# Kernel optimization log

Measured on AMD Instinct MI355X. Metric: run time of the kernel, lower is better.

## Reference

```python
import jax, jax.numpy as jnp
import numpy as np

EPS = 1e-5

def _conv(x, w, pad):
    # NCHW conv, stride 1, no bias
    return jax.lax.conv_general_dilated(x, w, (1, 1), [(pad, pad), (pad, pad)],
                                        dimension_numbers=('NCHW', 'OIHW', 'NCHW'))

def _bn(x, g, b, m, v):
    # inference-mode BatchNorm2d folded to scale/shift
    s = g * jax.lax.rsqrt(v + EPS)
    return x * s[None, :, None, None] + (b - m * s)[None, :, None, None]

def _cbr(x, w, g, b, m, v):
    # convolution helper module: 3x3 conv (pad 1, no bias) + BN + ReLU
    return jax.nn.relu(_bn(_conv(x, w, 1), g, b, m, v))


def setup_inputs() -> dict:
    key = jax.random.key(0)
    ks = iter(jax.random.split(key, 40))
    dim, mid, B, H, W = 256, 128, 4, 128, 128
    def conv_w(shape):
        fan = shape[1] * shape[2] * shape[3]
        return jax.random.normal(next(ks), shape, jnp.float32) / np.float32(np.sqrt(fan))
    def bn_p(c):
        return (jax.random.normal(next(ks), (c,), jnp.float32) * 0.1 + 1.0,
                jax.random.normal(next(ks), (c,), jnp.float32) * 0.1,
                jax.random.normal(next(ks), (c,), jnp.float32) * 0.1,
                jax.random.uniform(next(ks), (c,), jnp.float32, 0.5, 1.5))
    x = jax.random.normal(next(ks), (B, dim, H, W), jnp.float32)
    w_p1 = conv_w((mid, dim, 3, 3)); g_p1, b_p1, m_p1, v_p1 = bn_p(mid)
    w_p2 = conv_w((mid, dim, 3, 3)); g_p2, b_p2, m_p2, v_p2 = bn_p(mid)
    w_pc = conv_w((dim, mid, 3, 3)); g_pb, b_pb, m_pb, v_pb = bn_p(dim)
    w_c1 = conv_w((dim, dim, 1, 1)); g_b1, b_b1, m_b1, v_b1 = bn_p(dim)
    w_c2 = conv_w((dim, dim, 3, 3)); g_c2, b_c2, m_c2, v_c2 = bn_p(dim)
    return dict(x=x,
                w_p1=w_p1, g_p1=g_p1, b_p1=b_p1, m_p1=m_p1, v_p1=v_p1,
                w_p2=w_p2, g_p2=g_p2, b_p2=b_p2, m_p2=m_p2, v_p2=v_p2,
                w_pc=w_pc, g_pb=g_pb, b_pb=b_pb, m_pb=m_pb, v_pb=v_pb,
                w_c1=w_c1, g_b1=g_b1, b_b1=b_b1, m_b1=m_b1, v_b1=v_b1,
                w_c2=w_c2, g_c2=g_c2, b_c2=b_c2, m_c2=m_c2, v_c2=v_c2)


def reference(x, w_p1, g_p1, b_p1, m_p1, v_p1,
              w_p2, g_p2, b_p2, m_p2, v_p2,
              w_pc, g_pb, b_pb, m_pb, v_pb,
              w_c1, g_b1, b_b1, m_b1, v_b1,
              w_c2, g_c2, b_c2, m_c2, v_c2):
    p1 = _cbr(x, w_p1, g_p1, b_p1, m_p1, v_p1)          # [B,128,H,W]
    top = jax.lax.cummax(p1, axis=2, reverse=True)       # TopPool: max over rows below
    p2 = _cbr(x, w_p2, g_p2, b_p2, m_p2, v_p2)          # [B,128,H,W]
    left = jax.lax.cummax(p2, axis=3, reverse=True)      # LeftPool: max over cols to the right
    p_bn1 = _bn(_conv(top + left, w_pc, 1), g_pb, b_pb, m_pb, v_pb)  # [B,dim,H,W]
    bn1 = _bn(_conv(x, w_c1, 0), g_b1, b_b1, m_b1, v_b1)             # 1x1 skip branch
    relu1 = jax.nn.relu(p_bn1 + bn1)
    return _cbr(relu1, w_c2, g_c2, b_c2, m_c2, v_c2)
```

## Files before the change

kernel.cpp:

```cpp
#include <hip/hip_runtime.h>
#include <hip/hip_bf16.h>

#define HH 128
#define WW 128
#define BB 4
#define NPIX 16384
#define EPSV 1e-5f

using bfrag = __attribute__((ext_vector_type(8))) short;
using f32x4 = __attribute__((ext_vector_type(4))) float;
using us8   = __attribute__((ext_vector_type(8))) unsigned short;

__device__ __forceinline__ float bf2f(ushort u) {
  union { unsigned int i; float f; } x; x.i = ((unsigned int)u) << 16; return x.f;
}
__device__ __forceinline__ ushort f2bf(float f) {
  union { float f; unsigned int i; } x; x.f = f;
  unsigned int r = x.i + 0x7fffu + ((x.i >> 16) & 1u);
  return (ushort)(r >> 16);
}

#define GLOAD16(gsrc, ldst) \
  __builtin_amdgcn_global_load_lds( \
      (const __attribute__((address_space(1))) unsigned int*)(gsrc), \
      (__attribute__((address_space(3))) unsigned int*)(ldst), 16, 0, 0)

template<int CIN1, int TAPS1, int CIN2, int TAPS2, int EPI>
__global__ __launch_bounds__(256, 2)
void convgemm(const ushort* __restrict__ B1,
              const ushort* __restrict__ B2,
              const ushort* __restrict__ wR,
              const float*  __restrict__ tb,
              const float*  __restrict__ tb2,
              void*          __restrict__ outp,
              const ushort* __restrict__ zerop)
{
  __shared__ ushort lds[2][16384];
  constexpr int nch1 = CIN1 / 64;
  constexpr int nch2 = (CIN2 > 0) ? CIN2 / 64 : 0;
  constexpr int NCH  = TAPS1 * nch1 + TAPS2 * nch2;

  const int g  = blockIdx.x & 7;
  const int r  = blockIdx.x >> 3;
  const int bo = r >> 4;
  const int h  = g * 16 + (r & 15);
  const int o_base = (bo & 1) * 128;
  const int b  = bo >> 1;

  const int tid  = threadIdx.x;
  const int lane = tid & 63;
  const int wid  = tid >> 6;
  const int m0 = (wid >> 1) * 64;
  const int n0 = (wid & 1) * 64;

  f32x4 acc[4][4];
  #pragma unroll
  for (int i = 0; i < 4; ++i)
    #pragma unroll
    for (int j = 0; j < 4; ++j) acc[i][j] = (f32x4){0.f, 0.f, 0.f, 0.f};

  int rowB[4], ro1[4], ro2[4];
  #pragma unroll
  for (int s = 0; s < 4; ++s) {
    const int boff = (wid * 4 + s) * 1024 + lane * 16;
    rowB[s] = boff >> 7;
    const int sl8 = ((((boff >> 4) & 7) ^ (rowB[s] & 7)) << 3);
    ro1[s] = rowB[s] * CIN1 + sl8;
    ro2[s] = (CIN2 > 0) ? rowB[s] * CIN2 + sl8 : 0;
  }
  const size_t B1base = (size_t)b * NPIX * CIN1;
  const size_t B2base = (CIN2 > 0) ? (size_t)b * NPIX * CIN2 : 0;

  auto stage = [&](int t, int buf) {
    char* base = (char*)&lds[buf][0];
    const ushort* wsrc = wR + ((size_t)t * 256 + o_base) * 64;
    const ushort* bch;
    int zr; bool oob, ph2;
    if (CIN2 == 0 || t < TAPS1 * nch1) {
      const int tap = t / nch1, ch = t - tap * nch1;
      const int dy = (TAPS1 == 9) ? tap / 3 - 1 : 0;
      const int dx = (TAPS1 == 9) ? tap - (tap / 3) * 3 - 1 : 0;
      const int hy = h + dy;
      oob = (hy < 0) | (hy >= HH);
      zr  = (dx < 0) ? 0 : ((dx > 0) ? 127 : -1);
      bch = B1 + B1base + (size_t)(hy * WW + dx) * CIN1 + ch * 64;
      ph2 = false;
    } else {
      const int ch = t - TAPS1 * nch1;
      oob = false; zr = -1;
      bch = B2 + B2base + (size_t)(h * WW) * CIN2 + ch * 64;
      ph2 = true;
    }
    #pragma unroll
    for (int s = 0; s < 4; ++s) {
      const int off = (wid * 4 + s) * 1024;
      GLOAD16((const char*)wsrc + off + lane * 16, base + off);
      const int roff = ph2 ? ro2[s] : ro1[s];
      const ushort* bs = (oob || rowB[s] == zr) ? zerop : (bch + roff);
      GLOAD16(bs, base + 16384 + off);
    }
  };

  auto compute = [&](int buf) {
    const char* base = (const char*)&lds[buf][0];
    bfrag af[2][4], bfv[2][4];
    #pragma unroll
    for (int kc = 0; kc < 2; ++kc) {
      const int sw = ((((kc << 2) | (lane >> 4)) ^ (lane & 7)) << 4);
      #pragma unroll
      for (int mf = 0; mf < 4; ++mf)
        af[kc][mf] = *(const bfrag*)(base + (m0 + mf * 16 + (lane & 15)) * 128 + sw);
      #pragma unroll
      for (int nf = 0; nf < 4; ++nf)
        bfv[kc][nf] = *(const bfrag*)(base + 16384 + (n0 + nf * 16 + (lane & 15)) * 128 + sw);
    }
    __builtin_amdgcn_s_setprio(1);
    #pragma unroll
    for (int kc = 0; kc < 2; ++kc)
      #pragma unroll
      for (int mf = 0; mf < 4; ++mf)
        #pragma unroll
        for (int nf = 0; nf < 4; ++nf)
          acc[mf][nf] = __builtin_amdgcn_mfma_f32_16x16x32_bf16(
              af[kc][mf], bfv[kc][nf], acc[mf][nf], 0, 0, 0);
    __builtin_amdgcn_s_setprio(0);
  };

  stage(0, 0);
  int cur = 0;
  for (int t = 0; t < NCH; ++t) {
    asm volatile("s_waitcnt vmcnt(0)" ::: "memory");
    __builtin_amdgcn_s_barrier();
    __builtin_amdgcn_sched_barrier(0);
    if (t + 1 < NCH) stage(t + 1, cur ^ 1);
    compute(cur);
    cur ^= 1;
  }

  if (EPI == 4) {
    __syncthreads();
    ushort* ct = (ushort*)&lds[0][0];
    const int pl0 = n0 + (lane & 15);
    #pragma unroll
    for (int mf = 0; mf < 4; ++mf) {
      #pragma unroll
      for (int r2 = 0; r2 < 4; ++r2) {
        const int ol = m0 + mf * 16 + (lane >> 4) * 4 + r2;
        const int o  = o_base + ol;
        const float bias = tb[o] + tb2[o];
        #pragma unroll
        for (int nf = 0; nf < 4; ++nf)
          ct[(pl0 + nf * 16) * 136 + ol] =
              f2bf(fmaxf(acc[mf][nf][r2] + bias, 0.f));
      }
    }
    __syncthreads();
    const int p  = tid >> 1;
    const int hf = tid & 1;
    ushort* dst = (ushort*)outp +
                  ((size_t)b * NPIX + h * WW + p) * 256 + o_base + hf * 64;
    const ushort* src = ct + p * 136 + hf * 64;
    #pragma unroll
    for (int j = 0; j < 8; ++j)
      *(us8*)(dst + j * 8) = *(const us8*)(src + j * 8);
    return;
  }

  const int pc0 = h * WW + n0 + (lane & 15);
  #pragma unroll
  for (int mf = 0; mf < 4; ++mf) {
    #pragma unroll
    for (int r2 = 0; r2 < 4; ++r2) {
      const int o = o_base + m0 + mf * 16 + (lane >> 4) * 4 + r2;
      const float bias = tb[o];
      #pragma unroll
      for (int nf = 0; nf < 4; ++nf) {
        const int p = pc0 + nf * 16;
        float v = fmaxf(acc[mf][nf][r2] + bias, 0.f);
        const size_t oi = ((size_t)(b * 256 + o)) * NPIX + p;
        if (EPI == 0) ((ushort*)outp)[oi] = f2bf(v);
        else          ((float*)outp)[oi] = v;
      }
    }
  }
}

struct WSeg {
  const float *W, *g, *bb, *mm, *vv;
  ushort* dst; float* tb;
  int CIN, COUT, TAPS, o_off, cb, start, end;
};

__device__ __forceinline__ void wrepack_one(const WSeg& s, int e) {
  const int tap = e % s.TAPS;
  const int ci  = (e / s.TAPS) % s.CIN;
  const int o   = e / (s.TAPS * s.CIN);
  const int oi  = o + s.o_off;
  const float sc = s.g[o] * rsqrtf(s.vv[o] + EPSV);
  const int nch = s.CIN / 64;
  const int ch = ci >> 6, kl = ci & 63;
  const int slot = (kl >> 3) ^ (oi & 7);
  s.dst[(((size_t)((s.cb + tap * nch + ch) * s.COUT) + oi) << 6) +
        (slot << 3) + (kl & 7)] = f2bf(s.W[e] * sc);
  if (ci == 0 && tap == 0) s.tb[oi] = s.bb[o] - s.mm[o] * sc;
}

__global__ __launch_bounds__(256)
void wrepack_all(WSeg s0, WSeg s1, WSeg s2, WSeg s3, WSeg s4) {
  const int id = blockIdx.x * 256 + threadIdx.x;
  if (id < s0.end)      wrepack_one(s0, id - s0.start);
  else if (id < s1.end) wrepack_one(s1, id - s1.start);
  else if (id < s2.end) wrepack_one(s2, id - s2.start);
  else if (id < s3.end) wrepack_one(s3, id - s3.start);
  else if (id < s4.end) wrepack_one(s4, id - s4.start);
}

__global__ __launch_bounds__(256)
void repack_x(const float* __restrict__ x, ushort* __restrict__ xT)
{
  const int b  = blockIdx.z;
  const int cq = threadIdx.x >> 6;
  const int pg = threadIdx.x & 63;
  const int p0 = blockIdx.x * 256 + pg * 4;
  const size_t xb = (size_t)b * 256 * NPIX;
  ushort* ob = xT + ((size_t)b * NPIX + p0) * 256 + cq * 64;
  for (int cc = 0; cc < 64; cc += 8) {
    us8 v[4];
    #pragma unroll
    for (int j = 0; j < 8; ++j) {
      const float4 q = *(const float4*)&x[xb + (size_t)(cq * 64 + cc + j) * NPIX + p0];
      v[0][j] = f2bf(q.x); v[1][j] = f2bf(q.y);
      v[2][j] = f2bf(q.z); v[3][j] = f2bf(q.w);
    }
    #pragma unroll
    for (int k = 0; k < 4; ++k)
      *(us8*)(ob + (size_t)k * 256 + cc) = v[k];
  }
}

__global__ __launch_bounds__(256)
void sum_repack(const ushort* __restrict__ p12, ushort* __restrict__ sT)
{
  const int b  = blockIdx.z;
  const int cq = threadIdx.x >> 6;
  const int pg = threadIdx.x & 63;
  const int p0 = blockIdx.x * 256 + pg * 4;
  const size_t base = (size_t)b * 256 * NPIX;
  const ushort* P1 = p12 + base;
  const ushort* P2 = p12 + base + (size_t)128 * NPIX;
  ushort* ob = sT + ((size_t)b * NPIX + p0) * 128 + cq * 32;
  for (int cc = 0; cc < 32; cc += 8) {
    us8 v[4];
    #pragma unroll
    for (int j = 0; j < 8; ++j) {
      const size_t ci = (size_t)(cq * 32 + cc + j) * NPIX + p0;
      const ushort4 a = *(const ushort4*)&P1[ci];
      const ushort4 d = *(const ushort4*)&P2[ci];
      v[0][j] = f2bf(bf2f(a.x) + bf2f(d.x));
      v[1][j] = f2bf(bf2f(a.y) + bf2f(d.y));
      v[2][j] = f2bf(bf2f(a.z) + bf2f(d.z));
      v[3][j] = f2bf(bf2f(a.w) + bf2f(d.w));
    }
    #pragma unroll
    for (int k = 0; k < 4; ++k)
      *(us8*)(ob + (size_t)k * 128 + cc) = v[k];
  }
}

__global__ __launch_bounds__(256)
void scans(ushort* __restrict__ p)
{
  const int bid = blockIdx.x;
  if (bid < 256) {
    const int b = bid >> 6;
    const int c = (bid & 63) * 2 + (threadIdx.x >> 7);
    const int w = threadIdx.x & 127;
    ushort* base = p + ((size_t)(b * 256 + c)) * NPIX + w;
    float cur = bf2f(base[(HH - 1) * WW]);
    for (int hr = HH - 2; hr >= 0; --hr) {
      cur = fmaxf(cur, bf2f(base[hr * WW]));
      base[hr * WW] = f2bf(cur);
    }
  } else {
    const int lane = threadIdx.x & 63;
    const int rid  = (bid - 256) * 4 + (threadIdx.x >> 6);
    const int b = rid >> 14;
    const int rem = rid & 16383;
    const int c = rem >> 7, h = rem & 127;
    ushort* r = p + ((size_t)(b * 256 + 128 + c)) * NPIX + h * WW;
    const ushort2 u = ((const ushort2*)r)[lane];
    const float e0 = bf2f(u.x), e1 = bf2f(u.y);
    float m = fmaxf(e0, e1);
    #pragma unroll
    for (int off = 1; off < 64; off <<= 1) {
      const float o = __shfl_down(m, off, 64);
      if (lane + off < 64) m = fmaxf(m, o);
    }
    float s = __shfl_down(m, 1, 64);
    if (lane == 63) s = -3.4e38f;
    const float o1 = fmaxf(e1, s);
    const float o0 = fmaxf(e0, o1);
    ushort2 w2; w2.x = f2bf(o0); w2.y = f2bf(o1);
    ((ushort2*)r)[lane] = w2;
  }
}

extern "C" void kernel_launch(void* const* d_in, const int* in_sizes, int n_in,
                              void* d_out, int out_size, void* d_ws, size_t ws_size,
                              hipStream_t stream) {
  const float* x    = (const float*)d_in[0];
  const float* w_p1 = (const float*)d_in[1];
  const float* g_p1 = (const float*)d_in[2];
  const float* b_p1 = (const float*)d_in[3];
  const float* m_p1 = (const float*)d_in[4];
  const float* v_p1 = (const float*)d_in[5];
  const float* w_p2 = (const float*)d_in[6];
  const float* g_p2 = (const float*)d_in[7];
  const float* b_p2 = (const float*)d_in[8];
  const float* m_p2 = (const float*)d_in[9];
  const float* v_p2 = (const float*)d_in[10];
  const float* w_pc = (const float*)d_in[11];
  const float* g_pb = (const float*)d_in[12];
  const float* b_pb = (const float*)d_in[13];
  const float* m_pb = (const float*)d_in[14];
  const float* v_pb = (const float*)d_in[15];
  const float* w_c1 = (const float*)d_in[16];
  const float* g_b1 = (const float*)d_in[17];
  const float* b_b1 = (const float*)d_in[18];
  const float* m_b1 = (const float*)d_in[19];
  const float* v_b1 = (const float*)d_in[20];
  const float* w_c2 = (const float*)d_in[21];
  const float* g_c2 = (const float*)d_in[22];
  const float* b_c2 = (const float*)d_in[23];
  const float* m_c2 = (const float*)d_in[24];
  const float* v_c2 = (const float*)d_in[25];

  char* ws = (char*)d_ws;
  ushort* xT      = (ushort*)(ws + 0);
  ushort* p12     = (ushort*)(ws + 33554432);
  ushort* relu1T  = (ushort*)(ws + 33554432);
  ushort* sumT    = (ushort*)(ws + 67108864);
  ushort* wR_p12  = (ushort*)(ws + 100663296);
  ushort* wR_pcc1 = (ushort*)(ws + 101842944);
  ushort* wR_c2   = (ushort*)(ws + 102563840);
  float*  tb_p12  = (float*)(ws + 103743488);
  float*  tb_pc   = (float*)(ws + 103744512);
  float*  tb_c1   = (float*)(ws + 103745536);
  float*  tb_c2   = (float*)(ws + 103746560);
  ushort* zerop   = (ushort*)(ws + 103747584);

  hipMemsetAsync(zerop, 0, 256, stream);

  const int n_p  = 128 * 256 * 9;
  const int n_pc = 256 * 128 * 9;
  const int n_c1 = 256 * 256 * 1;
  const int n_c2 = 256 * 256 * 9;
  WSeg s0 = {w_p1, g_p1, b_p1, m_p1, v_p1, wR_p12, tb_p12, 256, 256, 9, 0, 0,
             0, n_p};
  WSeg s1 = {w_p2, g_p2, b_p2, m_p2, v_p2, wR_p12, tb_p12, 256, 256, 9, 128, 0,
             n_p, 2 * n_p};
  WSeg s2 = {w_pc, g_pb, b_pb, m_pb, v_pb, wR_pcc1, tb_pc, 128, 256, 9, 0, 0,
             2 * n_p, 2 * n_p + n_pc};
  WSeg s3 = {w_c1, g_b1, b_b1, m_b1, v_b1, wR_pcc1, tb_c1, 256, 256, 1, 0, 18,
             2 * n_p + n_pc, 2 * n_p + n_pc + n_c1};
  WSeg s4 = {w_c2, g_c2, b_c2, m_c2, v_c2, wR_c2, tb_c2, 256, 256, 9, 0, 0,
             2 * n_p + n_pc + n_c1, 2 * n_p + n_pc + n_c1 + n_c2};
  const int n_all = 2 * n_p + n_pc + n_c1 + n_c2;
  wrepack_all<<<dim3((n_all + 255) / 256), 256, 0, stream>>>(s0, s1, s2, s3, s4);

  repack_x<<<dim3(NPIX / 256, 1, BB), 256, 0, stream>>>(x, xT);

  convgemm<256, 9, 0, 0, 0><<<dim3(1024), 256, 0, stream>>>(
      xT, nullptr, wR_p12, tb_p12, nullptr, p12, zerop);

  scans<<<dim3(256 + 16384), 256, 0, stream>>>(p12);

  sum_repack<<<dim3(NPIX / 256, 1, BB), 256, 0, stream>>>(p12, sumT);

  convgemm<128, 9, 256, 1, 4><<<dim3(1024), 256, 0, stream>>>(
      sumT, xT, wR_pcc1, tb_pc, tb_c1, relu1T, zerop);

  convgemm<256, 9, 0, 0, 3><<<dim3(1024), 256, 0, stream>>>(
      relu1T, nullptr, wR_c2, tb_c2, nullptr, (void*)d_out, zerop);
}
```

Before: 300.2 us.

## Enlarge conv GEMM tile to 256 outputs x 2 rows with 512-thread blocks

Each convgemm block now computes all 256 output channels for two image rows (256 pixels) with 8 waves, and each wave holds a 128x64 accumulator tile. This halves redundant loads: weights are staged once per block instead of per half, and activations are reused across all output channels. Weight and activation staging is split into two phases, interleaved with the two MFMA halves and partial vmcnt waits, to overlap loads with compute. The larger LDS footprint (128KB) and doubled accumulators raise register and LDS pressure and cut the grid to 256 blocks, which lowers occupancy.

```diff
diff --git a/kernel.cpp b/kernel.cpp
--- a/kernel.cpp
+++ b/kernel.cpp
@@ -26,7 +26,7 @@
       (__attribute__((address_space(3))) unsigned int*)(ldst), 16, 0, 0)
 
 template<int CIN1, int TAPS1, int CIN2, int TAPS2, int EPI>
-__global__ __launch_bounds__(256, 2)
+__global__ __launch_bounds__(512, 2)
 void convgemm(const ushort* __restrict__ B1,
               const ushort* __restrict__ B2,
               const ushort* __restrict__ wR,
@@ -35,85 +35,98 @@
               void*          __restrict__ outp,
               const ushort* __restrict__ zerop)
 {
-  __shared__ ushort lds[2][16384];
+  __shared__ char ldsb[131072];
   constexpr int nch1 = CIN1 / 64;
   constexpr int nch2 = (CIN2 > 0) ? CIN2 / 64 : 0;
   constexpr int NCH  = TAPS1 * nch1 + TAPS2 * nch2;
 
-  const int g  = blockIdx.x & 7;
-  const int r  = blockIdx.x >> 3;
-  const int bo = r >> 4;
-  const int h  = g * 16 + (r & 15);
-  const int o_base = (bo & 1) * 128;
-  const int b  = bo >> 1;
+  const int nid = (blockIdx.x & 7) * 32 + (blockIdx.x >> 3);
+  const int b   = nid >> 6;
+  const int h2  = (nid & 63) * 2;
 
   const int tid  = threadIdx.x;
   const int lane = tid & 63;
   const int wid  = tid >> 6;
-  const int m0 = (wid >> 1) * 64;
-  const int n0 = (wid & 1) * 64;
-
-  f32x4 acc[4][4];
+  const int wc   = wid & 3;
+  const int m0   = (wid >> 2) * 128;
+  const int n0   = wc * 64;
+
+  f32x4 acc[8][4];
   #pragma unroll
-  for (int i = 0; i < 4; ++i)
+  for (int i = 0; i < 8; ++i)
     #pragma unroll
     for (int j = 0; j < 4; ++j) acc[i][j] = (f32x4){0.f, 0.f, 0.f, 0.f};
 
-  int rowB[4], ro1[4], ro2[4];
+  const int sl8 = (((tid & 7) ^ ((tid >> 3) & 7)) << 3);
+  int ro1[4], ro2[4], w_[4], prow_[4];
   #pragma unroll
   for (int s = 0; s < 4; ++s) {
-    const int boff = (wid * 4 + s) * 1024 + lane * 16;
-    rowB[s] = boff >> 7;
-    const int sl8 = ((((boff >> 4) & 7) ^ (rowB[s] & 7)) << 3);
-    ro1[s] = rowB[s] * CIN1 + sl8;
-    ro2[s] = (CIN2 > 0) ? rowB[s] * CIN2 + sl8 : 0;
+    const int rowB = s * 64 + (tid >> 3);
+    prow_[s] = rowB >> 7;
+    w_[s]    = rowB & 127;
+    ro1[s]   = (prow_[s] * WW + w_[s]) * CIN1 + sl8;
+    ro2[s]   = (CIN2 > 0) ? rowB * CIN2 + sl8 : 0;
   }
   const size_t B1base = (size_t)b * NPIX * CIN1;
   const size_t B2base = (CIN2 > 0) ? (size_t)b * NPIX * CIN2 : 0;
 
-  auto stage = [&](int t, int buf) {
-    char* base = (char*)&lds[buf][0];
-    const ushort* wsrc = wR + ((size_t)t * 256 + o_base) * 64;
-    const ushort* bch;
-    int zr; bool oob, ph2;
+  auto stageB = [&](int t, int buf) {
+    char* base = ldsb + buf * 65536 + 32768;
     if (CIN2 == 0 || t < TAPS1 * nch1) {
       const int tap = t / nch1, ch = t - tap * nch1;
       const int dy = (TAPS1 == 9) ? tap / 3 - 1 : 0;
       const int dx = (TAPS1 == 9) ? tap - (tap / 3) * 3 - 1 : 0;
-      const int hy = h + dy;
-      oob = (hy < 0) | (hy >= HH);
-      zr  = (dx < 0) ? 0 : ((dx > 0) ? 127 : -1);
-      bch = B1 + B1base + (size_t)(hy * WW + dx) * CIN1 + ch * 64;
-      ph2 = false;
+      const int hy0 = h2 + dy;
+      const bool oob0 = (hy0 < 0) | (hy0 > 127);
+      const bool oob1 = (hy0 + 1 < 0) | (hy0 + 1 > 127);
+      const int zr = (dx < 0) ? 0 : ((dx > 0) ? 127 : -1);
+      const ushort* bch = B1 + B1base + (size_t)(hy0 * WW + dx) * CIN1 + ch * 64;
+      #pragma unroll
+      for (int s = 0; s < 4; ++s) {
+        const bool bad = (prow_[s] ? oob1 : oob0) || (w_[s] == zr);
+        const ushort* src = bad ? zerop : (bch + ro1[s]);
+        GLOAD16(src, base + s * 8192 + tid * 16);
+      }
     } else {
       const int ch = t - TAPS1 * nch1;
-      oob = false; zr = -1;
-      bch = B2 + B2base + (size_t)(h * WW) * CIN2 + ch * 64;
-      ph2 = true;
-    }
-    #pragma unroll
-    for (int s = 0; s < 4; ++s) {
-      const int off = (wid * 4 + s) * 1024;
-      GLOAD16((const char*)wsrc + off + lane * 16, base + off);
-      const int roff = ph2 ? ro2[s] : ro1[s];
-      const ushort* bs = (oob || rowB[s] == zr) ? zerop : (bch + roff);
-      GLOAD16(bs, base + 16384 + off);
+      const ushort* bch = B2 + B2base + (size_t)(h2 * WW) * CIN2 + ch * 64;
+      #pragma unroll
+      for (int s = 0; s < 4; ++s)
+        GLOAD16(bch + ro2[s], base + s * 8192 + tid * 16);
     }
   };
 
-  auto compute = [&](int buf) {
-    const char* base = (const char*)&lds[buf][0];
-    bfrag af[2][4], bfv[2][4];
+  auto stageA = [&](int t, int buf) {
+    char* base = ldsb + buf * 65536;
+    const char* wsrc = (const char*)(wR + (size_t)t * (256 * 64));
+    GLOAD16(wsrc + 0 * 8192 + tid * 16, base + 0 * 8192 + tid * 16);
+    GLOAD16(wsrc + 2 * 8192 + tid * 16, base + 2 * 8192 + tid * 16);
+    GLOAD16(wsrc + 1 * 8192 + tid * 16, base + 1 * 8192 + tid * 16);
+    GLOAD16(wsrc + 3 * 8192 + tid * 16, base + 3 * 8192 + tid * 16);
+  };
+
+  stageB(0, 0);
+  stageA(0, 0);
+  int cur = 0;
+  for (int t = 0; t < NCH; ++t) {
+    const char* cbase = ldsb + cur * 65536;
+    asm volatile("s_waitcnt vmcnt(2)" ::: "memory");
+    __builtin_amdgcn_s_barrier();
+    __builtin_amdgcn_sched_barrier(0);
+    bfrag bf[2][4], af[2][4];
     #pragma unroll
     for (int kc = 0; kc < 2; ++kc) {
       const int sw = ((((kc << 2) | (lane >> 4)) ^ (lane & 7)) << 4);
       #pragma unroll
+      for (int nf = 0; nf < 4; ++nf)
+        bf[kc][nf] = *(const bfrag*)(cbase + 32768 +
+                        (n0 + nf * 16 + (lane & 15)) * 128 + sw);
+      #pragma unroll
       for (int mf = 0; mf < 4; ++mf)
-        af[kc][mf] = *(const bfrag*)(base + (m0 + mf * 16 + (lane & 15)) * 128 + sw);
-      #pragma unroll
-      for (int nf = 0; nf < 4; ++nf)
-        bfv[kc][nf] = *(const bfrag*)(base + 16384 + (n0 + nf * 16 + (lane & 15)) * 128 + sw);
-    }
+        af[kc][mf] = *(const bfrag*)(cbase +
+                        (m0 + mf * 16 + (lane & 15)) * 128 + sw);
+    }
+    if (t + 1 < NCH) stageB(t + 1, cur ^ 1);
     __builtin_amdgcn_s_setprio(1);
     #pragma unroll
     for (int kc = 0; kc < 2; ++kc)
@@ -122,62 +135,84 @@
         #pragma unroll
         for (int nf = 0; nf < 4; ++nf)
           acc[mf][nf] = __builtin_amdgcn_mfma_f32_16x16x32_bf16(
-              af[kc][mf], bfv[kc][nf], acc[mf][nf], 0, 0, 0);
+              af[kc][mf], bf[kc][nf], acc[mf][nf], 0, 0, 0);
     __builtin_amdgcn_s_setprio(0);
-  };
-
-  stage(0, 0);
-  int cur = 0;
-  for (int t = 0; t < NCH; ++t) {
-    asm volatile("s_waitcnt vmcnt(0)" ::: "memory");
+    __builtin_amdgcn_sched_barrier(0);
+    if (t + 1 < NCH) asm volatile("s_waitcnt vmcnt(4)" ::: "memory");
+    else             asm volatile("s_waitcnt vmcnt(0)" ::: "memory");
     __builtin_amdgcn_s_barrier();
     __builtin_amdgcn_sched_barrier(0);
-    if (t + 1 < NCH) stage(t + 1, cur ^ 1);
-    compute(cur);
-    cur ^= 1;
-  }
-
-  if (EPI == 4) {
-    __syncthreads();
-    ushort* ct = (ushort*)&lds[0][0];
-    const int pl0 = n0 + (lane & 15);
-    #pragma unroll
-    for (int mf = 0; mf < 4; ++mf) {
-      #pragma unroll
-      for (int r2 = 0; r2 < 4; ++r2) {
-        const int ol = m0 + mf * 16 + (lane >> 4) * 4 + r2;
-        const int o  = o_base + ol;
-        const float bias = tb[o] + tb2[o];
+    bfrag ag[2][4];
+    #pragma unroll
+    for (int kc = 0; kc < 2; ++kc) {
+      const int sw = ((((kc << 2) | (lane >> 4)) ^ (lane & 7)) << 4);
+      #pragma unroll
+      for (int mf = 0; mf < 4; ++mf)
+        ag[kc][mf] = *(const bfrag*)(cbase +
+                        (m0 + 64 + mf * 16 + (lane & 15)) * 128 + sw);
+    }
+    if (t + 1 < NCH) stageA(t + 1, cur ^ 1);
+    __builtin_amdgcn_s_setprio(1);
+    #pragma unroll
+    for (int kc = 0; kc < 2; ++kc)
+      #pragma unroll
+      for (int mf = 0; mf < 4; ++mf)
         #pragma unroll
         for (int nf = 0; nf < 4; ++nf)
-          ct[(pl0 + nf * 16) * 136 + ol] =
-              f2bf(fmaxf(acc[mf][nf][r2] + bias, 0.f));
+          acc[4 + mf][nf] = __builtin_amdgcn_mfma_f32_16x16x32_bf16(
+              ag[kc][mf], bf[kc][nf], acc[4 + mf][nf], 0, 0, 0);
+    __builtin_amdgcn_s_setprio(0);
+    __builtin_amdgcn_sched_barrier(0);
+    cur ^= 1;
+  }
+
+  if (EPI == 4) {
+    ushort* ct = (ushort*)ldsb;
+    #pragma unroll
+    for (int ph = 0; ph < 2; ++ph) {
+      __syncthreads();
+      if ((wc >> 1) == ph) {
+        const int lp0 = (wc & 1) * 64 + (lane & 15);
+        #pragma unroll
+        for (int mf = 0; mf < 8; ++mf) {
+          #pragma unroll
+          for (int r2 = 0; r2 < 4; ++r2) {
+            const int o = m0 + mf * 16 + (lane >> 4) * 4 + r2;
+            const float bias = tb[o] + tb2[o];
+            #pragma unroll
+            for (int nf = 0; nf < 4; ++nf)
+              ct[(lp0 + nf * 16) * 264 + o] =
+                  f2bf(fmaxf(acc[mf][nf][r2] + bias, 0.f));
+          }
+        }
       }
-    }
-    __syncthreads();
-    const int p  = tid >> 1;
-    const int hf = tid & 1;
-    ushort* dst = (ushort*)outp +
-                  ((size_t)b * NPIX + h * WW + p) * 256 + o_base + hf * 64;
-    const ushort* src = ct + p * 136 + hf * 64;
-    #pragma unroll
-    for (int j = 0; j < 8; ++j)
-      *(us8*)(dst + j * 8) = *(const us8*)(src + j * 8);
+      __syncthreads();
+      const int lp = tid >> 2;
+      const int q  = tid & 3;
+      ushort* dst = (ushort*)outp +
+          ((size_t)b * NPIX + (h2 + ph) * WW + lp) * 256 + q * 64;
+      const ushort* src = ct + lp * 264 + q * 64;
+      #pragma unroll
+      for (int j = 0; j < 8; ++j)
+        *(us8*)(dst + j * 8) = *(const us8*)(src + j * 8);
+    }
     return;
   }
 
-  const int pc0 = h * WW + n0 + (lane & 15);
+  const int prow = wc >> 1;
+  const int hout = h2 + prow;
+  const int wbase = (wc & 1) * 64 + (lane & 15);
   #pragma unroll
-  for (int mf = 0; mf < 4; ++mf) {
+  for (int mf = 0; mf < 8; ++mf) {
     #pragma unroll
     for (int r2 = 0; r2 < 4; ++r2) {
-      const int o = o_base + m0 + mf * 16 + (lane >> 4) * 4 + r2;
+      const int o = m0 + mf * 16 + (lane >> 4) * 4 + r2;
       const float bias = tb[o];
       #pragma unroll
       for (int nf = 0; nf < 4; ++nf) {
-        const int p = pc0 + nf * 16;
+        const int w = wbase + nf * 16;
         float v = fmaxf(acc[mf][nf][r2] + bias, 0.f);
-        const size_t oi = ((size_t)(b * 256 + o)) * NPIX + p;
+        const size_t oi = (((size_t)(b * 256 + o)) << 14) + hout * WW + w;
         if (EPI == 0) ((ushort*)outp)[oi] = f2bf(v);
         else          ((float*)outp)[oi] = v;
       }
@@ -370,16 +405,16 @@
 
   repack_x<<<dim3(NPIX / 256, 1, BB), 256, 0, stream>>>(x, xT);
 
-  convgemm<256, 9, 0, 0, 0><<<dim3(1024), 256, 0, stream>>>(
+  convgemm<256, 9, 0, 0, 0><<<dim3(256), 512, 0, stream>>>(
       xT, nullptr, wR_p12, tb_p12, nullptr, p12, zerop);
 
   scans<<<dim3(256 + 16384), 256, 0, stream>>>(p12);
 
   sum_repack<<<dim3(NPIX / 256, 1, BB), 256, 0, stream>>>(p12, sumT);
 
-  convgemm<128, 9, 256, 1, 4><<<dim3(1024), 256, 0, stream>>>(
+  convgemm<128, 9, 256, 1, 4><<<dim3(256), 512, 0, stream>>>(
       sumT, xT, wR_pcc1, tb_pc, tb_c1, relu1T, zerop);
 
-  convgemm<256, 9, 0, 0, 3><<<dim3(1024), 256, 0, stream>>>(
+  convgemm<256, 9, 0, 0, 3><<<dim3(256), 512, 0, stream>>>(
       relu1T, nullptr, wR_c2, tb_c2, nullptr, (void*)d_out, zerop);
 }
```

Result: faster. 287.1 us (-4.4%).

## Load weight fragments straight to registers and deepen activation LDS pipeline

Applied to the files above, without the earlier changes.

Weight (A) fragments for the next K-chunk are now loaded from global memory directly into registers, double-buffered across two register sets, instead of being staged through LDS. Activation (B) tiles are staged two chunks ahead into a 4-slot LDS ring, with partial vmcnt waits in place of full drains. The goal is to remove LDS traffic and bank pressure for the weights and to hide global latency behind more MFMA work. In exchange it raises register pressure, duplicates weight reads across waves that share m0, and makes the vmcnt counting fragile.

```diff
diff --git a/kernel.cpp b/kernel.cpp
--- a/kernel.cpp
+++ b/kernel.cpp
@@ -35,7 +35,7 @@
               void*          __restrict__ outp,
               const ushort* __restrict__ zerop)
 {
-  __shared__ ushort lds[2][16384];
+  __shared__ ushort lds[4][8192];
   constexpr int nch1 = CIN1 / 64;
   constexpr int nch2 = (CIN2 > 0) ? CIN2 / 64 : 0;
   constexpr int NCH  = TAPS1 * nch1 + TAPS2 * nch2;
@@ -62,7 +62,7 @@
   int rowB[4], ro1[4], ro2[4];
   #pragma unroll
   for (int s = 0; s < 4; ++s) {
-    const int boff = (wid * 4 + s) * 1024 + lane * 16;
+    const int boff = s * 4096 + tid * 16;
     rowB[s] = boff >> 7;
     const int sl8 = ((((boff >> 4) & 7) ^ (rowB[s] & 7)) << 3);
     ro1[s] = rowB[s] * CIN1 + sl8;
@@ -71,11 +71,9 @@
   const size_t B1base = (size_t)b * NPIX * CIN1;
   const size_t B2base = (CIN2 > 0) ? (size_t)b * NPIX * CIN2 : 0;
 
-  auto stage = [&](int t, int buf) {
+  auto stageB = [&](int t, int buf) {
     char* base = (char*)&lds[buf][0];
-    const ushort* wsrc = wR + ((size_t)t * 256 + o_base) * 64;
-    const ushort* bch;
-    int zr; bool oob, ph2;
+    const ushort* bch; int zr; bool oob, ph2;
     if (CIN2 == 0 || t < TAPS1 * nch1) {
       const int tap = t / nch1, ch = t - tap * nch1;
       const int dy = (TAPS1 == 9) ? tap / 3 - 1 : 0;
@@ -93,48 +91,63 @@
     }
     #pragma unroll
     for (int s = 0; s < 4; ++s) {
-      const int off = (wid * 4 + s) * 1024;
-      GLOAD16((const char*)wsrc + off + lane * 16, base + off);
       const int roff = ph2 ? ro2[s] : ro1[s];
       const ushort* bs = (oob || rowB[s] == zr) ? zerop : (bch + roff);
-      GLOAD16(bs, base + 16384 + off);
+      GLOAD16(bs, base + s * 4096 + tid * 16);
     }
   };
 
-  auto compute = [&](int buf) {
-    const char* base = (const char*)&lds[buf][0];
-    bfrag af[2][4], bfv[2][4];
-    #pragma unroll
-    for (int kc = 0; kc < 2; ++kc) {
-      const int sw = ((((kc << 2) | (lane >> 4)) ^ (lane & 7)) << 4);
-      #pragma unroll
-      for (int mf = 0; mf < 4; ++mf)
-        af[kc][mf] = *(const bfrag*)(base + (m0 + mf * 16 + (lane & 15)) * 128 + sw);
-      #pragma unroll
-      for (int nf = 0; nf < 4; ++nf)
-        bfv[kc][nf] = *(const bfrag*)(base + 16384 + (n0 + nf * 16 + (lane & 15)) * 128 + sw);
-    }
-    __builtin_amdgcn_s_setprio(1);
-    #pragma unroll
-    for (int kc = 0; kc < 2; ++kc)
-      #pragma unroll
-      for (int mf = 0; mf < 4; ++mf)
-        #pragma unroll
-        for (int nf = 0; nf < 4; ++nf)
-          acc[mf][nf] = __builtin_amdgcn_mfma_f32_16x16x32_bf16(
-              af[kc][mf], bfv[kc][nf], acc[mf][nf], 0, 0, 0);
-    __builtin_amdgcn_s_setprio(0);
-  };
-
-  stage(0, 0);
-  int cur = 0;
-  for (int t = 0; t < NCH; ++t) {
-    asm volatile("s_waitcnt vmcnt(0)" ::: "memory");
-    __builtin_amdgcn_s_barrier();
-    __builtin_amdgcn_sched_barrier(0);
-    if (t + 1 < NCH) stage(t + 1, cur ^ 1);
-    compute(cur);
-    cur ^= 1;
+#define LOADA(t_, A_) do { \
+    const char* wsrc_ = (const char*)wR + (size_t)(t_) * 32768 + \
+                        (size_t)(o_base + m0 + (lane & 15)) * 128; \
+    _Pragma("unroll") \
+    for (int kc_ = 0; kc_ < 2; ++kc_) { \
+      const int sw_ = ((((kc_ << 2) | (lane >> 4)) ^ (lane & 7)) << 4); \
+      _Pragma("unroll") \
+      for (int mf_ = 0; mf_ < 4; ++mf_) \
+        A_[kc_][mf_] = *(const bfrag*)(wsrc_ + mf_ * 2048 + sw_); \
+    } } while (0)
+
+#define BODY(t_, Acur_, Anext_) do { \
+    if ((t_) + 1 < NCH) { asm volatile("s_waitcnt vmcnt(12)" ::: "memory"); } \
+    else                { asm volatile("s_waitcnt vmcnt(8)"  ::: "memory"); } \
+    __builtin_amdgcn_s_barrier(); \
+    __builtin_amdgcn_sched_barrier(0); \
+    if ((t_) + 1 < NCH) LOADA((t_) + 1, Anext_); \
+    __builtin_amdgcn_sched_barrier(0); \
+    if ((t_) + 2 < NCH) stageB((t_) + 2, ((t_) + 2) & 3); \
+    const char* bbase_ = (const char*)&lds[(t_) & 3][0]; \
+    bfrag bf_[2][4]; \
+    _Pragma("unroll") \
+    for (int kc_ = 0; kc_ < 2; ++kc_) { \
+      const int sw_ = ((((kc_ << 2) | (lane >> 4)) ^ (lane & 7)) << 4); \
+      _Pragma("unroll") \
+      for (int nf_ = 0; nf_ < 4; ++nf_) \
+        bf_[kc_][nf_] = *(const bfrag*)(bbase_ + \
+                          (n0 + nf_ * 16 + (lane & 15)) * 128 + sw_); \
+    } \
+    __builtin_amdgcn_s_setprio(1); \
+    _Pragma("unroll") \
+    for (int kc_ = 0; kc_ < 2; ++kc_) \
+      _Pragma("unroll") \
+      for (int mf_ = 0; mf_ < 4; ++mf_) \
+        _Pragma("unroll") \
+        for (int nf_ = 0; nf_ < 4; ++nf_) \
+          acc[mf_][nf_] = __builtin_amdgcn_mfma_f32_16x16x32_bf16( \
+              Acur_[kc_][mf_], bf_[kc_][nf_], acc[mf_][nf_], 0, 0, 0); \
+    __builtin_amdgcn_s_setprio(0); \
+    __builtin_amdgcn_sched_barrier(0); \
+  } while (0)
+
+  bfrag Aa[2][4], Ab[2][4];
+  stageB(0, 0);
+  __builtin_amdgcn_sched_barrier(0);
+  LOADA(0, Aa);
+  __builtin_amdgcn_sched_barrier(0);
+  stageB(1, 1);
+  for (int t = 0; t < NCH; t += 2) {
+    BODY(t, Aa, Ab);
+    BODY(t + 1, Ab, Aa);
   }
 
   if (EPI == 4) {
@@ -183,6 +196,8 @@
       }
     }
   }
+#undef BODY
+#undef LOADA
 }
 
 struct WSeg {
```

Measured after the change: 342.5 us. 14.1% more time.

## Emit pool convs channel-last and fuse scans with sum into transposed buffers

Applied to the files above, without the earlier changes.

The first pool conv now writes its output in pixel-major (channel-last) layout through the EPI 4 epilogue, using a zero second bias. This replaces the in-place NCHW scans and the separate sum_repack transpose with two scan kernels: one runs the top cummax into a topT buffer, the other runs the left cummax and adds topT directly into sumT. The GEMM loop is also reordered so the LDS fragment reads happen before the next stage's global loads are issued. The new scans use only 512 blocks of 128 threads, each running a serial loop of 128 steps, so parallelism is low, and topT adds an extra buffer round trip.

```diff
diff --git a/kernel.cpp b/kernel.cpp
--- a/kernel.cpp
+++ b/kernel.cpp
@@ -101,8 +101,13 @@
     }
   };
 
-  auto compute = [&](int buf) {
-    const char* base = (const char*)&lds[buf][0];
+  stage(0, 0);
+  int cur = 0;
+  for (int t = 0; t < NCH; ++t) {
+    asm volatile("s_waitcnt vmcnt(0)" ::: "memory");
+    __builtin_amdgcn_s_barrier();
+    __builtin_amdgcn_sched_barrier(0);
+    const char* base = (const char*)&lds[cur][0];
     bfrag af[2][4], bfv[2][4];
     #pragma unroll
     for (int kc = 0; kc < 2; ++kc) {
@@ -114,6 +119,7 @@
       for (int nf = 0; nf < 4; ++nf)
         bfv[kc][nf] = *(const bfrag*)(base + 16384 + (n0 + nf * 16 + (lane & 15)) * 128 + sw);
     }
+    if (t + 1 < NCH) stage(t + 1, cur ^ 1);
     __builtin_amdgcn_s_setprio(1);
     #pragma unroll
     for (int kc = 0; kc < 2; ++kc)
@@ -124,16 +130,6 @@
           acc[mf][nf] = __builtin_amdgcn_mfma_f32_16x16x32_bf16(
               af[kc][mf], bfv[kc][nf], acc[mf][nf], 0, 0, 0);
     __builtin_amdgcn_s_setprio(0);
-  };
-
-  stage(0, 0);
-  int cur = 0;
-  for (int t = 0; t < NCH; ++t) {
-    asm volatile("s_waitcnt vmcnt(0)" ::: "memory");
-    __builtin_amdgcn_s_barrier();
-    __builtin_amdgcn_sched_barrier(0);
-    if (t + 1 < NCH) stage(t + 1, cur ^ 1);
-    compute(cur);
     cur ^= 1;
   }
 
@@ -238,70 +234,35 @@
   }
 }
 
-__global__ __launch_bounds__(256)
-void sum_repack(const ushort* __restrict__ p12, ushort* __restrict__ sT)
+__global__ __launch_bounds__(128)
+void scan_top(const ushort* __restrict__ p12T, ushort* __restrict__ topT)
 {
-  const int b  = blockIdx.z;
-  const int cq = threadIdx.x >> 6;
-  const int pg = threadIdx.x & 63;
-  const int p0 = blockIdx.x * 256 + pg * 4;
-  const size_t base = (size_t)b * 256 * NPIX;
-  const ushort* P1 = p12 + base;
-  const ushort* P2 = p12 + base + (size_t)128 * NPIX;
-  ushort* ob = sT + ((size_t)b * NPIX + p0) * 128 + cq * 32;
-  for (int cc = 0; cc < 32; cc += 8) {
-    us8 v[4];
-    #pragma unroll
-    for (int j = 0; j < 8; ++j) {
-      const size_t ci = (size_t)(cq * 32 + cc + j) * NPIX + p0;
-      const ushort4 a = *(const ushort4*)&P1[ci];
-      const ushort4 d = *(const ushort4*)&P2[ci];
-      v[0][j] = f2bf(bf2f(a.x) + bf2f(d.x));
-      v[1][j] = f2bf(bf2f(a.y) + bf2f(d.y));
-      v[2][j] = f2bf(bf2f(a.z) + bf2f(d.z));
-      v[3][j] = f2bf(bf2f(a.w) + bf2f(d.w));
-    }
-    #pragma unroll
-    for (int k = 0; k < 4; ++k)
-      *(us8*)(ob + (size_t)k * 128 + cc) = v[k];
-  }
-}
-
-__global__ __launch_bounds__(256)
-void scans(ushort* __restrict__ p)
+  const int b = blockIdx.x >> 7;
+  const int w = blockIdx.x & 127;
+  const int c = threadIdx.x;
+  const size_t ib = (size_t)b * NPIX;
+  float cur = -3.4e38f;
+  for (int h = HH - 1; h >= 0; --h) {
+    const size_t p = ib + h * WW + w;
+    cur = fmaxf(cur, bf2f(p12T[p * 256 + c]));
+    topT[p * 128 + c] = f2bf(cur);
+  }
+}
+
+__global__ __launch_bounds__(128)
+void scan_left_sum(const ushort* __restrict__ p12T,
+                   const ushort* __restrict__ topT,
+                   ushort* __restrict__ sumT)
 {
-  const int bid = blockIdx.x;
-  if (bid < 256) {
-    const int b = bid >> 6;
-    const int c = (bid & 63) * 2 + (threadIdx.x >> 7);
-    const int w = threadIdx.x & 127;
-    ushort* base = p + ((size_t)(b * 256 + c)) * NPIX + w;
-    float cur = bf2f(base[(HH - 1) * WW]);
-    for (int hr = HH - 2; hr >= 0; --hr) {
-      cur = fmaxf(cur, bf2f(base[hr * WW]));
-      base[hr * WW] = f2bf(cur);
-    }
-  } else {
-    const int lane = threadIdx.x & 63;
-    const int rid  = (bid - 256) * 4 + (threadIdx.x >> 6);
-    const int b = rid >> 14;
-    const int rem = rid & 16383;
-    const int c = rem >> 7, h = rem & 127;
-    ushort* r = p + ((size_t)(b * 256 + 128 + c)) * NPIX + h * WW;
-    const ushort2 u = ((const ushort2*)r)[lane];
-    const float e0 = bf2f(u.x), e1 = bf2f(u.y);
-    float m = fmaxf(e0, e1);
-    #pragma unroll
-    for (int off = 1; off < 64; off <<= 1) {
-      const float o = __shfl_down(m, off, 64);
-      if (lane + off < 64) m = fmaxf(m, o);
-    }
-    float s = __shfl_down(m, 1, 64);
-    if (lane == 63) s = -3.4e38f;
-    const float o1 = fmaxf(e1, s);
-    const float o0 = fmaxf(e0, o1);
-    ushort2 w2; w2.x = f2bf(o0); w2.y = f2bf(o1);
-    ((ushort2*)r)[lane] = w2;
+  const int b = blockIdx.x >> 7;
+  const int h = blockIdx.x & 127;
+  const int c = threadIdx.x;
+  const size_t ib = (size_t)b * NPIX + h * WW;
+  float cur = -3.4e38f;
+  for (int w = WW - 1; w >= 0; --w) {
+    const size_t p = ib + w;
+    cur = fmaxf(cur, bf2f(p12T[p * 256 + 128 + c]));
+    sumT[p * 128 + c] = f2bf(cur + bf2f(topT[p * 128 + c]));
   }
 }
 
@@ -337,9 +298,10 @@
 
   char* ws = (char*)d_ws;
   ushort* xT      = (ushort*)(ws + 0);
-  ushort* p12     = (ushort*)(ws + 33554432);
+  ushort* p12T    = (ushort*)(ws + 33554432);
   ushort* relu1T  = (ushort*)(ws + 33554432);
   ushort* sumT    = (ushort*)(ws + 67108864);
+  ushort* topT    = (ushort*)(ws + 83886080);
   ushort* wR_p12  = (ushort*)(ws + 100663296);
   ushort* wR_pcc1 = (ushort*)(ws + 101842944);
   ushort* wR_c2   = (ushort*)(ws + 102563840);
@@ -348,8 +310,9 @@
   float*  tb_c1   = (float*)(ws + 103745536);
   float*  tb_c2   = (float*)(ws + 103746560);
   ushort* zerop   = (ushort*)(ws + 103747584);
-
-  hipMemsetAsync(zerop, 0, 256, stream);
+  float*  tb_zero = (float*)(ws + 103747840);
+
+  hipMemsetAsync(zerop, 0, 256 + 1024, stream);
 
   const int n_p  = 128 * 256 * 9;
   const int n_pc = 256 * 128 * 9;
@@ -370,12 +333,11 @@
 
   repack_x<<<dim3(NPIX / 256, 1, BB), 256, 0, stream>>>(x, xT);
 
-  convgemm<256, 9, 0, 0, 0><<<dim3(1024), 256, 0, stream>>>(
-      xT, nullptr, wR_p12, tb_p12, nullptr, p12, zerop);
-
-  scans<<<dim3(256 + 16384), 256, 0, stream>>>(p12);
-
-  sum_repack<<<dim3(NPIX / 256, 1, BB), 256, 0, stream>>>(p12, sumT);
+  convgemm<256, 9, 0, 0, 4><<<dim3(1024), 256, 0, stream>>>(
+      xT, nullptr, wR_p12, tb_p12, tb_zero, p12T, zerop);
+
+  scan_top<<<dim3(BB * 128), 128, 0, stream>>>(p12T, topT);
+  scan_left_sum<<<dim3(BB * 128), 128, 0, stream>>>(p12T, topT, sumT);
 
   convgemm<128, 9, 256, 1, 4><<<dim3(1024), 256, 0, stream>>>(
       sumT, xT, wR_pcc1, tb_pc, tb_c1, relu1T, zerop);
```

Result: no change. 299.1 us (-0.3%).
